# Kernel optimization log

Hardware: AMD Instinct MI355X
Metric: run time of the kernel (lower is better)

The kernel has to match this reference:

```python
import jax, jax.numpy as jnp
import numpy as np

N = 50000          # nodes
E = 800000         # edges
B = 256            # graphs in batch
D = 128            # emb_dim
L = 4              # num_layer
K = 3              # Chebyshev order (self._k)
TASKS = 128        # num_tasks
ATOM_VOCAB = 100
BOND_VOCAB = 5
EPS = 1e-5


def setup_inputs() -> dict:
    key = jax.random.key(0)
    ks = jax.random.split(key, 16)
    h_idx = jax.random.randint(ks[0], (N, 9), 0, ATOM_VOCAB)
    e_idx = jax.random.randint(ks[1], (E, 3), 0, BOND_VOCAB)
    src = jax.random.randint(ks[2], (E,), 0, N)
    dst = jax.random.randint(ks[3], (E,), 0, N)
    node2graph = jnp.sort(jax.random.randint(ks[4], (N,), 0, B))
    s = 0.02
    atom_emb = jax.random.normal(ks[5], (9, ATOM_VOCAB, D), jnp.float32) * s
    bond_emb = jax.random.normal(ks[6], (3, BOND_VOCAB, D), jnp.float32) * s
    layer_W = jax.random.normal(ks[7], (L, K * D, D), jnp.float32) / np.sqrt(K * D)
    layer_gamma = jnp.ones((L, D), jnp.float32)
    layer_beta = jnp.zeros((L, D), jnp.float32)
    ro_W0 = jax.random.normal(ks[8], (D, D // 2), jnp.float32) / np.sqrt(D)
    ro_b0 = jnp.zeros((D // 2,), jnp.float32)
    ro_W1 = jax.random.normal(ks[9], (D // 2, D // 4), jnp.float32) / np.sqrt(D // 2)
    ro_b1 = jnp.zeros((D // 4,), jnp.float32)
    ro_W2 = jax.random.normal(ks[10], (D // 4, TASKS), jnp.float32) / np.sqrt(D // 4)
    ro_b2 = jnp.zeros((TASKS,), jnp.float32)
    return dict(h_idx=h_idx, e_idx=e_idx, src=src, dst=dst, node2graph=node2graph,
                atom_emb=atom_emb, bond_emb=bond_emb, layer_W=layer_W,
                layer_gamma=layer_gamma, layer_beta=layer_beta,
                ro_W0=ro_W0, ro_b0=ro_b0, ro_W1=ro_W1, ro_b1=ro_b1,
                ro_W2=ro_W2, ro_b2=ro_b2)


def _batchnorm(h, gamma, beta):
    # training-mode BatchNorm1d over node dim (biased variance, as torch)
    mu = h.mean(0)
    var = h.var(0)
    return (h - mu) * jax.lax.rsqrt(var + EPS) * gamma + beta


def reference(h_idx, e_idx, src, dst, node2graph, atom_emb, bond_emb,
              layer_W, layer_gamma, layer_beta,
              ro_W0, ro_b0, ro_W1, ro_b1, ro_W2, ro_b2):
    # Atom/Bond encoders: sum of per-feature embeddings
    h = sum(atom_emb[f][h_idx[:, f]] for f in range(9))          # [N, D]
    e = sum(bond_emb[f][e_idx[:, f]] for f in range(3))          # [E, D] (unused by ChebLayer)

    # symmetric degree normalization from in-degrees (dst counts), clamp min 1
    deg = jax.ops.segment_sum(jnp.ones((E,), h.dtype), dst, num_segments=N)
    d_sqrt = jnp.power(jnp.maximum(deg, 1.0), -0.5)[:, None]      # [N, 1]

    def prop(x):
        m = (x * d_sqrt)[src]                                     # [E, D]
        agg = jax.ops.segment_sum(m, dst, num_segments=N)         # [N, D]
        return agg * d_sqrt

    re_norm = 1.0  # 2 / lambda_max, lambda_max hard-coded to 2

    for l in range(L):
        h_in = h
        X0 = h
        h1 = prop(X0)
        X1 = -re_norm * h1 + X0 * (re_norm - 1.0)
        h2 = prop(X1)
        X2 = -2.0 * re_norm * h2 + X1 * 2.0 * (re_norm - 1.0) - X0
        Xt = jnp.concatenate((X0, X1, X2), axis=1)                # [N, 3D]
        h = Xt @ layer_W[l]                                       # [N, D]
        h = _batchnorm(h, layer_gamma[l], layer_beta[l])
        h = jax.nn.relu(h)
        h = h_in + h                                              # residual (in==out dims)

    # mean pooling over nodes per graph
    sums = jax.ops.segment_sum(h, node2graph, num_segments=B)     # [B, D]
    cnts = jax.ops.segment_sum(jnp.ones((N,), h.dtype), node2graph, num_segments=B)
    hg = sums / jnp.maximum(cnts, 1.0)[:, None]

    # MLPReadout: D -> D/2 -> D/4 -> TASKS
    y = jax.nn.relu(hg @ ro_W0 + ro_b0)
    y = jax.nn.relu(y @ ro_W1 + ro_b1)
    return y @ ro_W2 + ro_b2                                      # [B, TASKS]
```

## Files before the change

### kernel.cpp

```cpp
#include <hip/hip_runtime.h>

#define N_NODES 50000
#define N_EDGES 800000
#define BGRAPH  256
#define DIM     128
#define NLAYER  4
#define EPS     1e-5f
#define NBUCK   ((N_NODES + 255) / 256)
#define WSZ     (384 * DIM)
#define EB_PER  4096

typedef _Float16 half8_t __attribute__((ext_vector_type(8)));
typedef float    f32x4   __attribute__((ext_vector_type(4)));

__global__ __launch_bounds__(1024) void bcount_kernel(const int* __restrict__ dst,
                                                      int* __restrict__ bcnt) {
    __shared__ int h[NBUCK];
    int t = threadIdx.x;
    if (t < NBUCK) h[t] = 0;
    __syncthreads();
    for (int e = blockIdx.x * 1024 + t; e < N_EDGES; e += gridDim.x * 1024)
        atomicAdd(&h[dst[e] >> 8], 1);
    __syncthreads();
    if (t < NBUCK && h[t]) atomicAdd(&bcnt[t], h[t]);
}

__global__ void bscan_kernel(const int* __restrict__ bcnt, int* __restrict__ boff,
                             int* __restrict__ bcur) {
    __shared__ int lds[256];
    int t = threadIdx.x;
    int v = (t < NBUCK) ? bcnt[t] : 0;
    lds[t] = v;
    __syncthreads();
    for (int off = 1; off < 256; off <<= 1) {
        int u = (t >= off) ? lds[t - off] : 0;
        __syncthreads();
        lds[t] += u;
        __syncthreads();
    }
    if (t < NBUCK) { int ex = lds[t] - v; boff[t] = ex; bcur[t] = ex; }
    if (t == NBUCK - 1) boff[NBUCK] = lds[t];
}

__global__ __launch_bounds__(1024) void bexpand_kernel(const int* __restrict__ src,
                                                       const int* __restrict__ dst,
                                                       int* __restrict__ bcur,
                                                       int2* __restrict__ ebuf) {
    __shared__ int2 stage[EB_PER];
    __shared__ int hist[NBUCK];
    __shared__ int lofs[NBUCK];
    __shared__ int lcur[NBUCK];
    __shared__ int gbase[NBUCK];
    __shared__ int s[256];
    int t = threadIdx.x;
    int e0 = blockIdx.x * EB_PER;
    int total = N_EDGES - e0; if (total > EB_PER) total = EB_PER;
    if (t < NBUCK) hist[t] = 0;
    __syncthreads();
    int mys[4], myd[4], myb[4];
#pragma unroll
    for (int j = 0; j < 4; ++j) {
        int e = e0 + t + j * 1024;
        if (e < N_EDGES) {
            mys[j] = src[e]; myd[j] = dst[e]; myb[j] = myd[j] >> 8;
            atomicAdd(&hist[myb[j]], 1);
        } else myb[j] = -1;
    }
    __syncthreads();
    if (t < 256) s[t] = (t < NBUCK) ? hist[t] : 0;
    __syncthreads();
    for (int off = 1; off < 256; off <<= 1) {
        int u = 0;
        if (t < 256 && t >= off) u = s[t - off];
        __syncthreads();
        if (t < 256) s[t] += u;
        __syncthreads();
    }
    if (t < NBUCK) {
        int v = hist[t];
        int ex = s[t] - v;
        lofs[t] = ex; lcur[t] = ex;
        gbase[t] = (v > 0) ? atomicAdd(&bcur[t], v) : 0;
    }
    __syncthreads();
#pragma unroll
    for (int j = 0; j < 4; ++j) if (myb[j] >= 0) {
        int p = atomicAdd(&lcur[myb[j]], 1);
        stage[p] = make_int2(mys[j], myd[j]);
    }
    __syncthreads();
    for (int i = t; i < total; i += 1024) {
        int2 p = stage[i];
        int bu = p.y >> 8;
        ebuf[gbase[bu] + (i - lofs[bu])] = p;
    }
}

__global__ __launch_bounds__(256) void bbuild_kernel(const int2* __restrict__ ebuf,
                                                     const int* __restrict__ boff,
                                                     int* __restrict__ row_ptr,
                                                     float* __restrict__ dsq,
                                                     float* __restrict__ invd,
                                                     int* __restrict__ csr_src) {
    __shared__ int hist[256];
    __shared__ int s[256];
    __shared__ int lcur[256];
    int b = blockIdx.x, t = threadIdx.x;
    int base = boff[b], cnt = boff[b + 1] - base;
    int node0 = b << 8;
    hist[t] = 0;
    __syncthreads();
    for (int i = t; i < cnt; i += 256)
        atomicAdd(&hist[ebuf[base + i].y & 255], 1);
    __syncthreads();
    int v = hist[t];
    s[t] = v;
    __syncthreads();
    for (int off = 1; off < 256; off <<= 1) {
        int u = (t >= off) ? s[t - off] : 0;
        __syncthreads();
        s[t] += u;
        __syncthreads();
    }
    int excl = s[t] - v;
    lcur[t] = excl;
    int n = node0 + t;
    if (n < N_NODES) {
        row_ptr[n] = base + excl;
        float d = (float)(v < 1 ? 1 : v);
        dsq[n] = 1.0f / sqrtf(d);
        invd[n] = sqrtf(d);
        if (n == N_NODES - 1) row_ptr[N_NODES] = base + excl + v;
    }
    __syncthreads();
    for (int i = t; i < cnt; i += 256) {
        int2 p = ebuf[base + i];
        int slot = atomicAdd(&lcur[p.y & 255], 1);
        csr_src[base + slot] = p.x;
    }
}

__global__ void wcvt_kernel(const float* __restrict__ W, _Float16* __restrict__ Wp) {
    int idx = blockIdx.x * blockDim.x + threadIdx.x;
    if (idx >= NLAYER * WSZ) return;
    int l = idx / WSZ;
    int r = idx - l * WSZ;
    int j = r & 7, lane = (r >> 3) & 63, t = (r >> 9) & 7, kb = r >> 12;
    int k = (kb << 5) + ((lane >> 4) << 3) + j;
    int n = (t << 4) + (lane & 15);
    Wp[idx] = (_Float16)W[l * WSZ + (k << 7) + n];
}

__global__ void encode_kernel(const int* __restrict__ h_idx,
                              const float* __restrict__ atom_emb,
                              const float* __restrict__ dsq,
                              float* __restrict__ H, _Float16* __restrict__ H16s) {
    int n = blockIdx.x;
    int d = threadIdx.x;
    float acc = 0.0f;
#pragma unroll
    for (int f = 0; f < 9; ++f) {
        int idx = h_idx[n * 9 + f];
        acc += atom_emb[(f * 100 + idx) * DIM + d];
    }
    H[n * DIM + d] = acc;
    H16s[n * DIM + d] = (_Float16)(acc * dsq[n]);
}

#define PGROUPS 16
#define ACC8(r) { _Pragma("unroll") for (int jj = 0; jj < 8; ++jj) acc[jj] += (float)(r)[jj]; }
__global__ void prop_kernel(const int* __restrict__ row_ptr, const int* __restrict__ csr_src,
                            const float* __restrict__ dsq,
                            const _Float16* __restrict__ Gin, const float* __restrict__ X0,
                            float alpha, float beta, _Float16* __restrict__ Gout) {
    int n = blockIdx.x * PGROUPS + (threadIdx.x >> 4);
    if (n >= N_NODES) return;
    int q = (threadIdx.x & 15) << 3;
    const _Float16* gq = Gin + q;
    int i = row_ptr[n], endp = row_ptr[n + 1];
    float acc[8];
#pragma unroll
    for (int j = 0; j < 8; ++j) acc[j] = 0.f;

    if (i + 8 <= endp) {
        half8_t A[8];
        int idx[8];
#pragma unroll
        for (int j = 0; j < 8; ++j) idx[j] = csr_src[i + j];
#pragma unroll
        for (int j = 0; j < 8; ++j) A[j] = *(const half8_t*)&gq[(size_t)idx[j] * DIM];
        i += 8;
        for (; i + 8 <= endp; i += 8) {
            half8_t B[8];
            int id2[8];
#pragma unroll
            for (int j = 0; j < 8; ++j) id2[j] = csr_src[i + j];
#pragma unroll
            for (int j = 0; j < 8; ++j) B[j] = *(const half8_t*)&gq[(size_t)id2[j] * DIM];
#pragma unroll
            for (int j = 0; j < 8; ++j) ACC8(A[j]);
#pragma unroll
            for (int j = 0; j < 8; ++j) A[j] = B[j];
        }
#pragma unroll
        for (int j = 0; j < 8; ++j) ACC8(A[j]);
    }
    if (i + 4 <= endp) {
        int s0 = csr_src[i], s1 = csr_src[i+1], s2 = csr_src[i+2], s3 = csr_src[i+3];
        half8_t r0 = *(const half8_t*)&gq[(size_t)s0 * DIM];
        half8_t r1 = *(const half8_t*)&gq[(size_t)s1 * DIM];
        half8_t r2 = *(const half8_t*)&gq[(size_t)s2 * DIM];
        half8_t r3 = *(const half8_t*)&gq[(size_t)s3 * DIM];
        ACC8(r0); ACC8(r1); ACC8(r2); ACC8(r3);
        i += 4;
    }
    for (; i < endp; ++i) {
        int s = csr_src[i];
        half8_t r = *(const half8_t*)&gq[(size_t)s * DIM];
        ACC8(r);
    }

    float g = dsq[n];
    float a = alpha * g;
    half8_t out;
    if (beta != 0.0f) {
        const float* x0p = &X0[(size_t)n * DIM + q];
        float4 xa = *(const float4*)x0p;
        float4 xb = *(const float4*)(x0p + 4);
        float x0v[8] = {xa.x, xa.y, xa.z, xa.w, xb.x, xb.y, xb.z, xb.w};
#pragma unroll
        for (int j = 0; j < 8; ++j)
            out[j] = (_Float16)((a * acc[j] + beta * x0v[j]) * g);
    } else {
#pragma unroll
        for (int j = 0; j < 8; ++j)
            out[j] = (_Float16)(a * acc[j] * g);
    }
    *(half8_t*)&Gout[(size_t)n * DIM + q] = out;
}

__global__ __launch_bounds__(256) void gemm_kernel(
        const _Float16* __restrict__ X0s, const _Float16* __restrict__ X1s,
        const _Float16* __restrict__ X2s, const float* __restrict__ invd,
        const _Float16* __restrict__ Wp,
        _Float16* __restrict__ Out16, float* __restrict__ stats) {
    const int tid  = threadIdx.x;
    const int wave = tid >> 6;
    const int lane = tid & 63;
    const int quad = lane >> 4;
    const int l15  = lane & 15;
    const int row0 = blockIdx.x * 128 + wave * 32;
    const int rA = row0 + l15;
    const int rB = row0 + 16 + l15;
    const int rAc = (rA < N_NODES) ? rA : (N_NODES - 1);
    const int rBc = (rB < N_NODES) ? rB : (N_NODES - 1);
    const _Float16 h0 = (_Float16)((rA < N_NODES) ? invd[rA] : 0.0f);
    const _Float16 h1 = (_Float16)((rB < N_NODES) ? invd[rB] : 0.0f);

    f32x4 acc0[8], acc1[8];
#pragma unroll
    for (int t = 0; t < 8; ++t) {
        acc0[t] = (f32x4){0.f, 0.f, 0.f, 0.f};
        acc1[t] = (f32x4){0.f, 0.f, 0.f, 0.f};
    }

    const _Float16* bufs[3] = {X0s, X1s, X2s};

    for (int kb = 0; kb < 12; ++kb) {
        const _Float16* Xb = bufs[kb >> 2];
        const int c0 = ((kb & 3) << 5) + (quad << 3);
        half8_t a0 = *(const half8_t*)&Xb[(size_t)rAc * DIM + c0];
        half8_t a1 = *(const half8_t*)&Xb[(size_t)rBc * DIM + c0];
#pragma unroll
        for (int j = 0; j < 8; ++j) { a0[j] = a0[j] * h0; a1[j] = a1[j] * h1; }
        const _Float16* wl = Wp + (size_t)(((kb << 3) << 6) + lane) * 8;
#pragma unroll
        for (int t = 0; t < 8; ++t) {
            half8_t b = *(const half8_t*)&wl[t << 9];
            acc0[t] = __builtin_amdgcn_mfma_f32_16x16x32_f16(a0, b, acc0[t], 0, 0, 0);
            acc1[t] = __builtin_amdgcn_mfma_f32_16x16x32_f16(a1, b, acc1[t], 0, 0, 0);
        }
    }

    __shared__ float sred[4][DIM];
    __shared__ float s2red[4][DIM];
#pragma unroll
    for (int t = 0; t < 8; ++t) {
        const int c = (t << 4) + l15;
        float s = 0.f, s2 = 0.f;
#pragma unroll
        for (int reg = 0; reg < 4; ++reg) {
            float v0 = acc0[t][reg];
            float v1 = acc1[t][reg];
            s += v0 + v1; s2 += v0 * v0 + v1 * v1;
            int r0r = row0 + (quad << 2) + reg;
            int r1r = r0r + 16;
            if (r0r < N_NODES) Out16[(size_t)r0r * DIM + c] = (_Float16)v0;
            if (r1r < N_NODES) Out16[(size_t)r1r * DIM + c] = (_Float16)v1;
        }
        s  += __shfl_xor(s, 16);  s  += __shfl_xor(s, 32);
        s2 += __shfl_xor(s2, 16); s2 += __shfl_xor(s2, 32);
        if (quad == 0) { sred[wave][c] = s; s2red[wave][c] = s2; }
    }
    __syncthreads();
    if (tid < DIM) {
        float s = 0.f, s2 = 0.f;
#pragma unroll
        for (int w = 0; w < 4; ++w) { s += sred[w][tid]; s2 += s2red[w][tid]; }
        atomicAdd(&stats[tid], s);
        atomicAdd(&stats[DIM + tid], s2);
    }
}

__global__ void bnapply_kernel(const _Float16* __restrict__ Out16, const float* __restrict__ stats,
                               const float* __restrict__ gamma, const float* __restrict__ beta,
                               const float* __restrict__ dsq,
                               float* __restrict__ H, _Float16* __restrict__ H16s) {
    int idx = blockIdx.x * blockDim.x + threadIdx.x;
    if (idx >= N_NODES * DIM) return;
    int d = idx & 127;
    int n = idx >> 7;
    const float invN = 1.0f / (float)N_NODES;
    float mu  = stats[d] * invN;
    float var = stats[DIM + d] * invN - mu * mu;
    float sc  = (1.0f / sqrtf(var + EPS)) * gamma[d];
    float sh  = beta[d] - mu * sc;
    float v = (float)Out16[idx] * sc + sh;
    float h = H[idx] + fmaxf(v, 0.0f);
    H[idx] = h;
    H16s[idx] = (_Float16)(h * dsq[n]);
}

#define PCHUNK 64
__global__ void pool_kernel(const float* __restrict__ H, const int* __restrict__ n2g,
                            float* __restrict__ sums, float* __restrict__ cnts) {
    int d = threadIdx.x;
    int r0 = blockIdx.x * PCHUNK;
    int rend = r0 + PCHUNK; if (rend > N_NODES) rend = N_NODES;
    if (r0 >= N_NODES) return;
    float acc = 0.0f;
    int cur = n2g[r0];
    int runlen = 0;
    for (int r = r0; r < rend; ++r) {
        int g = n2g[r];
        if (g != cur) {
            atomicAdd(&sums[cur * DIM + d], acc);
            if (d == 0) atomicAdd(&cnts[cur], (float)runlen);
            acc = 0.0f; runlen = 0; cur = g;
        }
        acc += H[r * DIM + d];
        runlen++;
    }
    atomicAdd(&sums[cur * DIM + d], acc);
    if (d == 0) atomicAdd(&cnts[cur], (float)runlen);
}

__global__ void mlp_kernel(const float* __restrict__ sums, const float* __restrict__ cnts,
                           const float* __restrict__ W0, const float* __restrict__ b0,
                           const float* __restrict__ W1, const float* __restrict__ b1,
                           const float* __restrict__ W2, const float* __restrict__ b2,
                           float* __restrict__ out) {
    __shared__ float hg[DIM];
    __shared__ float y0[64];
    __shared__ float y1[32];
    int g = blockIdx.x;
    int t = threadIdx.x;
    float c = cnts[g]; if (c < 1.0f) c = 1.0f;
    hg[t] = sums[g * DIM + t] / c;
    __syncthreads();
    if (t < 64) {
        float acc = b0[t];
        for (int k = 0; k < 128; ++k) acc += hg[k] * W0[k * 64 + t];
        y0[t] = fmaxf(acc, 0.0f);
    }
    __syncthreads();
    if (t < 32) {
        float acc = b1[t];
        for (int k = 0; k < 64; ++k) acc += y0[k] * W1[k * 32 + t];
        y1[t] = fmaxf(acc, 0.0f);
    }
    __syncthreads();
    {
        float acc = b2[t];
        for (int k = 0; k < 32; ++k) acc += y1[k] * W2[k * 128 + t];
        out[g * DIM + t] = acc;
    }
}

extern "C" void kernel_launch(void* const* d_in, const int* in_sizes, int n_in,
                              void* d_out, int out_size, void* d_ws, size_t ws_size,
                              hipStream_t stream) {
    const int*   h_idx = (const int*)d_in[0];
    const int*   src   = (const int*)d_in[2];
    const int*   dst   = (const int*)d_in[3];
    const int*   n2g   = (const int*)d_in[4];
    const float* atom_emb = (const float*)d_in[5];
    const float* layer_W  = (const float*)d_in[7];
    const float* gamma    = (const float*)d_in[8];
    const float* beta     = (const float*)d_in[9];
    const float* W0 = (const float*)d_in[10];
    const float* b0 = (const float*)d_in[11];
    const float* W1 = (const float*)d_in[12];
    const float* b1 = (const float*)d_in[13];
    const float* W2 = (const float*)d_in[14];
    const float* b2 = (const float*)d_in[15];

    const size_t ND = (size_t)N_NODES * DIM;

    float*    H    = (float*)d_ws;
    _Float16* H16s = (_Float16*)(H + ND);
    _Float16* A16s = H16s + ND;
    _Float16* B16s = A16s + ND;
    _Float16* Out16 = B16s + ND;
    int2*     ebuf  = (int2*)Out16;
    _Float16* Wpack = Out16 + ND;
    float* dsq  = (float*)(Wpack + NLAYER * WSZ);
    float* invd = dsq + N_NODES;
    int*   row_ptr = (int*)(invd + N_NODES);
    int*   csr_src = row_ptr + N_NODES + 1;
    int*   bcnt = csr_src + N_EDGES;
    int*   boff = bcnt + NBUCK;
    int*   bcur = boff + NBUCK + 1;
    float* stats = (float*)(bcur + NBUCK);
    float* psums = stats + 2 * DIM;
    float* pcnts = psums + BGRAPH * DIM;

    hipMemsetAsync(bcnt, 0, NBUCK * sizeof(int), stream);
    bcount_kernel<<<128, 1024, 0, stream>>>(dst, bcnt);
    bscan_kernel<<<1, 256, 0, stream>>>(bcnt, boff, bcur);
    bexpand_kernel<<<(N_EDGES + EB_PER - 1) / EB_PER, 1024, 0, stream>>>(src, dst, bcur, ebuf);
    bbuild_kernel<<<NBUCK, 256, 0, stream>>>(ebuf, boff, row_ptr, dsq, invd, csr_src);
    wcvt_kernel<<<(NLAYER * WSZ + 255) / 256, 256, 0, stream>>>(layer_W, Wpack);

    encode_kernel<<<N_NODES, DIM, 0, stream>>>(h_idx, atom_emb, dsq, H, H16s);

    const int propGrid = (N_NODES + PGROUPS - 1) / PGROUPS;
    const int gemmGrid = (N_NODES + 127) / 128;
    for (int l = 0; l < NLAYER; ++l) {
        prop_kernel<<<propGrid, 256, 0, stream>>>(row_ptr, csr_src, dsq, H16s, H, -1.0f, 0.0f, A16s);
        prop_kernel<<<propGrid, 256, 0, stream>>>(row_ptr, csr_src, dsq, A16s, H, -2.0f, -1.0f, B16s);

        hipMemsetAsync(stats, 0, 2 * DIM * sizeof(float), stream);
        gemm_kernel<<<gemmGrid, 256, 0, stream>>>(H16s, A16s, B16s, invd,
                                                  Wpack + (size_t)l * WSZ, Out16, stats);

        bnapply_kernel<<<((int)ND + 255) / 256, 256, 0, stream>>>(Out16, stats,
                                                  gamma + l * DIM, beta + l * DIM, dsq, H, H16s);
    }

    hipMemsetAsync(psums, 0, (BGRAPH * DIM + BGRAPH) * sizeof(float), stream);
    pool_kernel<<<(N_NODES + PCHUNK - 1) / PCHUNK, DIM, 0, stream>>>(H, n2g, psums, pcnts);
    mlp_kernel<<<BGRAPH, DIM, 0, stream>>>(psums, pcnts, W0, b0, W1, b1, W2, b2, (float*)d_out);
}
```

Baseline: 642.6 us.

## Store residual state in fp16, software-pipeline GEMM loads, merge stats memsets

The fp32 residual buffer H becomes fp16. This halves its traffic in encode, prop (X0 read), bnapply and pool, at the cost of accumulating residual rounding error over the layers. The GEMM kernel now prefetches the next k-block's A and B fragments into registers while the current MFMAs run. The prop inner loop is narrowed from 8-wide to 4-wide gather batches. Per-layer stats memsets are replaced by one up-front memset of per-layer stats slots plus the pooling buffers.

```diff
diff --git a/kernel.cpp b/kernel.cpp
--- a/kernel.cpp
+++ b/kernel.cpp
@@ -154,7 +154,7 @@
 __global__ void encode_kernel(const int* __restrict__ h_idx,
                               const float* __restrict__ atom_emb,
                               const float* __restrict__ dsq,
-                              float* __restrict__ H, _Float16* __restrict__ H16s) {
+                              _Float16* __restrict__ H16, _Float16* __restrict__ H16s) {
     int n = blockIdx.x;
     int d = threadIdx.x;
     float acc = 0.0f;
@@ -163,7 +163,7 @@
         int idx = h_idx[n * 9 + f];
         acc += atom_emb[(f * 100 + idx) * DIM + d];
     }
-    H[n * DIM + d] = acc;
+    H16[n * DIM + d] = (_Float16)acc;
     H16s[n * DIM + d] = (_Float16)(acc * dsq[n]);
 }
 
@@ -171,7 +171,7 @@
 #define ACC8(r) { _Pragma("unroll") for (int jj = 0; jj < 8; ++jj) acc[jj] += (float)(r)[jj]; }
 __global__ void prop_kernel(const int* __restrict__ row_ptr, const int* __restrict__ csr_src,
                             const float* __restrict__ dsq,
-                            const _Float16* __restrict__ Gin, const float* __restrict__ X0,
+                            const _Float16* __restrict__ Gin, const _Float16* __restrict__ X0,
                             float alpha, float beta, _Float16* __restrict__ Gout) {
     int n = blockIdx.x * PGROUPS + (threadIdx.x >> 4);
     if (n >= N_NODES) return;
@@ -183,29 +183,23 @@
     for (int j = 0; j < 8; ++j) acc[j] = 0.f;
 
     if (i + 8 <= endp) {
-        half8_t A[8];
-        int idx[8];
-#pragma unroll
-        for (int j = 0; j < 8; ++j) idx[j] = csr_src[i + j];
-#pragma unroll
-        for (int j = 0; j < 8; ++j) A[j] = *(const half8_t*)&gq[(size_t)idx[j] * DIM];
-        i += 8;
-        for (; i + 8 <= endp; i += 8) {
-            half8_t B[8];
-            int id2[8];
-#pragma unroll
-            for (int j = 0; j < 8; ++j) id2[j] = csr_src[i + j];
-#pragma unroll
-            for (int j = 0; j < 8; ++j) B[j] = *(const half8_t*)&gq[(size_t)id2[j] * DIM];
-#pragma unroll
-            for (int j = 0; j < 8; ++j) ACC8(A[j]);
-#pragma unroll
-            for (int j = 0; j < 8; ++j) A[j] = B[j];
-        }
-#pragma unroll
-        for (int j = 0; j < 8; ++j) ACC8(A[j]);
-    }
-    if (i + 4 <= endp) {
+        int s0 = csr_src[i], s1 = csr_src[i+1], s2 = csr_src[i+2], s3 = csr_src[i+3];
+        half8_t a0 = *(const half8_t*)&gq[(size_t)s0 * DIM];
+        half8_t a1 = *(const half8_t*)&gq[(size_t)s1 * DIM];
+        half8_t a2 = *(const half8_t*)&gq[(size_t)s2 * DIM];
+        half8_t a3 = *(const half8_t*)&gq[(size_t)s3 * DIM];
+        i += 4;
+        for (; i + 4 <= endp; i += 4) {
+            int t0 = csr_src[i], t1 = csr_src[i+1], t2 = csr_src[i+2], t3 = csr_src[i+3];
+            half8_t b0 = *(const half8_t*)&gq[(size_t)t0 * DIM];
+            half8_t b1 = *(const half8_t*)&gq[(size_t)t1 * DIM];
+            half8_t b2 = *(const half8_t*)&gq[(size_t)t2 * DIM];
+            half8_t b3 = *(const half8_t*)&gq[(size_t)t3 * DIM];
+            ACC8(a0); ACC8(a1); ACC8(a2); ACC8(a3);
+            a0 = b0; a1 = b1; a2 = b2; a3 = b3;
+        }
+        ACC8(a0); ACC8(a1); ACC8(a2); ACC8(a3);
+    } else if (i + 4 <= endp) {
         int s0 = csr_src[i], s1 = csr_src[i+1], s2 = csr_src[i+2], s3 = csr_src[i+3];
         half8_t r0 = *(const half8_t*)&gq[(size_t)s0 * DIM];
         half8_t r1 = *(const half8_t*)&gq[(size_t)s1 * DIM];
@@ -224,13 +218,10 @@
     float a = alpha * g;
     half8_t out;
     if (beta != 0.0f) {
-        const float* x0p = &X0[(size_t)n * DIM + q];
-        float4 xa = *(const float4*)x0p;
-        float4 xb = *(const float4*)(x0p + 4);
-        float x0v[8] = {xa.x, xa.y, xa.z, xa.w, xb.x, xb.y, xb.z, xb.w};
+        half8_t x0 = *(const half8_t*)&X0[(size_t)n * DIM + q];
 #pragma unroll
         for (int j = 0; j < 8; ++j)
-            out[j] = (_Float16)((a * acc[j] + beta * x0v[j]) * g);
+            out[j] = (_Float16)((a * acc[j] + beta * (float)x0[j]) * g);
     } else {
 #pragma unroll
         for (int j = 0; j < 8; ++j)
@@ -266,19 +257,40 @@
 
     const _Float16* bufs[3] = {X0s, X1s, X2s};
 
+    half8_t a0c, a1c, a0n, a1n, bc[8], bn[8];
+    {
+        const _Float16* Xb = bufs[0];
+        const int c0 = (quad << 3);
+        a0c = *(const half8_t*)&Xb[(size_t)rAc * DIM + c0];
+        a1c = *(const half8_t*)&Xb[(size_t)rBc * DIM + c0];
+        const _Float16* wl = Wp + (size_t)lane * 8;
+#pragma unroll
+        for (int t = 0; t < 8; ++t) bc[t] = *(const half8_t*)&wl[t << 9];
+    }
+
     for (int kb = 0; kb < 12; ++kb) {
-        const _Float16* Xb = bufs[kb >> 2];
-        const int c0 = ((kb & 3) << 5) + (quad << 3);
-        half8_t a0 = *(const half8_t*)&Xb[(size_t)rAc * DIM + c0];
-        half8_t a1 = *(const half8_t*)&Xb[(size_t)rBc * DIM + c0];
-#pragma unroll
-        for (int j = 0; j < 8; ++j) { a0[j] = a0[j] * h0; a1[j] = a1[j] * h1; }
-        const _Float16* wl = Wp + (size_t)(((kb << 3) << 6) + lane) * 8;
+        if (kb < 11) {
+            const int kn = kb + 1;
+            const _Float16* Xb = bufs[kn >> 2];
+            const int c0 = ((kn & 3) << 5) + (quad << 3);
+            a0n = *(const half8_t*)&Xb[(size_t)rAc * DIM + c0];
+            a1n = *(const half8_t*)&Xb[(size_t)rBc * DIM + c0];
+            const _Float16* wl = Wp + (size_t)((kn << 9) + lane) * 8;
+#pragma unroll
+            for (int t = 0; t < 8; ++t) bn[t] = *(const half8_t*)&wl[t << 9];
+        }
+        half8_t a0, a1;
+#pragma unroll
+        for (int j = 0; j < 8; ++j) { a0[j] = a0c[j] * h0; a1[j] = a1c[j] * h1; }
 #pragma unroll
         for (int t = 0; t < 8; ++t) {
-            half8_t b = *(const half8_t*)&wl[t << 9];
-            acc0[t] = __builtin_amdgcn_mfma_f32_16x16x32_f16(a0, b, acc0[t], 0, 0, 0);
-            acc1[t] = __builtin_amdgcn_mfma_f32_16x16x32_f16(a1, b, acc1[t], 0, 0, 0);
+            acc0[t] = __builtin_amdgcn_mfma_f32_16x16x32_f16(a0, bc[t], acc0[t], 0, 0, 0);
+            acc1[t] = __builtin_amdgcn_mfma_f32_16x16x32_f16(a1, bc[t], acc1[t], 0, 0, 0);
+        }
+        if (kb < 11) {
+            a0c = a0n; a1c = a1n;
+#pragma unroll
+            for (int t = 0; t < 8; ++t) bc[t] = bn[t];
         }
     }
 
@@ -315,7 +327,7 @@
 __global__ void bnapply_kernel(const _Float16* __restrict__ Out16, const float* __restrict__ stats,
                                const float* __restrict__ gamma, const float* __restrict__ beta,
                                const float* __restrict__ dsq,
-                               float* __restrict__ H, _Float16* __restrict__ H16s) {
+                               _Float16* __restrict__ H16, _Float16* __restrict__ H16s) {
     int idx = blockIdx.x * blockDim.x + threadIdx.x;
     if (idx >= N_NODES * DIM) return;
     int d = idx & 127;
@@ -326,13 +338,13 @@
     float sc  = (1.0f / sqrtf(var + EPS)) * gamma[d];
     float sh  = beta[d] - mu * sc;
     float v = (float)Out16[idx] * sc + sh;
-    float h = H[idx] + fmaxf(v, 0.0f);
-    H[idx] = h;
+    float h = (float)H16[idx] + fmaxf(v, 0.0f);
+    H16[idx] = (_Float16)h;
     H16s[idx] = (_Float16)(h * dsq[n]);
 }
 
 #define PCHUNK 64
-__global__ void pool_kernel(const float* __restrict__ H, const int* __restrict__ n2g,
+__global__ void pool_kernel(const _Float16* __restrict__ H16, const int* __restrict__ n2g,
                             float* __restrict__ sums, float* __restrict__ cnts) {
     int d = threadIdx.x;
     int r0 = blockIdx.x * PCHUNK;
@@ -348,7 +360,7 @@
             if (d == 0) atomicAdd(&cnts[cur], (float)runlen);
             acc = 0.0f; runlen = 0; cur = g;
         }
-        acc += H[r * DIM + d];
+        acc += (float)H16[(size_t)r * DIM + d];
         runlen++;
     }
     atomicAdd(&sums[cur * DIM + d], acc);
@@ -407,8 +419,8 @@
 
     const size_t ND = (size_t)N_NODES * DIM;
 
-    float*    H    = (float*)d_ws;
-    _Float16* H16s = (_Float16*)(H + ND);
+    _Float16* H16  = (_Float16*)d_ws;
+    _Float16* H16s = H16 + ND;
     _Float16* A16s = H16s + ND;
     _Float16* B16s = A16s + ND;
     _Float16* Out16 = B16s + ND;
@@ -421,9 +433,12 @@
     int*   bcnt = csr_src + N_EDGES;
     int*   boff = bcnt + NBUCK;
     int*   bcur = boff + NBUCK + 1;
-    float* stats = (float*)(bcur + NBUCK);
-    float* psums = stats + 2 * DIM;
+    float* stats4 = (float*)(bcur + NBUCK);
+    float* psums = stats4 + NLAYER * 2 * DIM;
     float* pcnts = psums + BGRAPH * DIM;
+
+    hipMemsetAsync(stats4, 0,
+                   (NLAYER * 2 * DIM + BGRAPH * DIM + BGRAPH) * sizeof(float), stream);
 
     hipMemsetAsync(bcnt, 0, NBUCK * sizeof(int), stream);
     bcount_kernel<<<128, 1024, 0, stream>>>(dst, bcnt);
@@ -432,23 +447,22 @@
     bbuild_kernel<<<NBUCK, 256, 0, stream>>>(ebuf, boff, row_ptr, dsq, invd, csr_src);
     wcvt_kernel<<<(NLAYER * WSZ + 255) / 256, 256, 0, stream>>>(layer_W, Wpack);
 
-    encode_kernel<<<N_NODES, DIM, 0, stream>>>(h_idx, atom_emb, dsq, H, H16s);
+    encode_kernel<<<N_NODES, DIM, 0, stream>>>(h_idx, atom_emb, dsq, H16, H16s);
 
     const int propGrid = (N_NODES + PGROUPS - 1) / PGROUPS;
     const int gemmGrid = (N_NODES + 127) / 128;
     for (int l = 0; l < NLAYER; ++l) {
-        prop_kernel<<<propGrid, 256, 0, stream>>>(row_ptr, csr_src, dsq, H16s, H, -1.0f, 0.0f, A16s);
-        prop_kernel<<<propGrid, 256, 0, stream>>>(row_ptr, csr_src, dsq, A16s, H, -2.0f, -1.0f, B16s);
-
-        hipMemsetAsync(stats, 0, 2 * DIM * sizeof(float), stream);
+        prop_kernel<<<propGrid, 256, 0, stream>>>(row_ptr, csr_src, dsq, H16s, H16, -1.0f, 0.0f, A16s);
+        prop_kernel<<<propGrid, 256, 0, stream>>>(row_ptr, csr_src, dsq, A16s, H16, -2.0f, -1.0f, B16s);
+
+        float* stats = stats4 + l * 2 * DIM;
         gemm_kernel<<<gemmGrid, 256, 0, stream>>>(H16s, A16s, B16s, invd,
                                                   Wpack + (size_t)l * WSZ, Out16, stats);
 
         bnapply_kernel<<<((int)ND + 255) / 256, 256, 0, stream>>>(Out16, stats,
-                                                  gamma + l * DIM, beta + l * DIM, dsq, H, H16s);
-    }
-
-    hipMemsetAsync(psums, 0, (BGRAPH * DIM + BGRAPH) * sizeof(float), stream);
-    pool_kernel<<<(N_NODES + PCHUNK - 1) / PCHUNK, DIM, 0, stream>>>(H, n2g, psums, pcnts);
+                                                  gamma + l * DIM, beta + l * DIM, dsq, H16, H16s);
+    }
+
+    pool_kernel<<<(N_NODES + PCHUNK - 1) / PCHUNK, DIM, 0, stream>>>(H16, n2g, psums, pcnts);
     mlp_kernel<<<BGRAPH, DIM, 0, stream>>>(psums, pcnts, W0, b0, W1, b1, W2, b2, (float*)d_out);
 }
```

Result: faster. 576.4 us (-10.3%).
